# Kernel tuning notes

Hardware: AMD Instinct MI355X
Metric: run time of the kernel (lower is better)

## Reference

```python
import jax, jax.numpy as jnp
import numpy as np

DIV_VAL = 11.313708498984761  # sqrt(128), the softmax temperature used as div_val


def setup_inputs() -> dict:
    key = jax.random.key(0)
    kq, kk, kv = jax.random.split(key, 3)
    B, Lq, Lk, D = 16, 4096, 4096, 128
    return {
        "query": jax.random.normal(kq, (B, Lq, D), dtype=jnp.float32),
        "key": jax.random.normal(kk, (B, Lk, D), dtype=jnp.float32),
        "value": jax.random.normal(kv, (B, Lk, D), dtype=jnp.float32),
    }


def reference(query, key, value):
    # qk = Q @ K^T, scaled by 1/div_val  -> [B, Lq, Lk]
    scaled_qk = jnp.einsum("bqd,bkd->bqk", query, key) / DIV_VAL
    # numerically stable softmax over last axis; dropout is identity (eval / p=0)
    attn = jax.nn.softmax(scaled_qk, axis=-1)
    # output = attn @ V -> [B, Lq, Dv]
    return jnp.einsum("bqk,bkd->bqd", attn, value)
```

## Files before the change

kernel.cpp:

```cpp
#include <hip/hip_runtime.h>

#define B_  16
#define L_  4096
#define D_  128
#define NT  (L_ / 64)

typedef __attribute__((ext_vector_type(8)))  __bf16 bf16x8;
typedef __attribute__((ext_vector_type(2)))  __bf16 bf16x2;
typedef __attribute__((ext_vector_type(16))) float  f32x16;
typedef __attribute__((ext_vector_type(4)))  float  f32x4;
typedef __attribute__((ext_vector_type(4)))  int    i32x4;
typedef __attribute__((ext_vector_type(8)))  unsigned short u16x8;
typedef __attribute__((ext_vector_type(4)))  unsigned short u16x4;

#ifndef __has_builtin
#define __has_builtin(x) 0
#endif
#if __has_builtin(__builtin_amdgcn_permlane32_swap)
#define HAVE_PLSWAP 1
#else
#define HAVE_PLSWAP 0
#endif

__device__ __forceinline__ unsigned short f2bf(float f){
  unsigned u = __builtin_bit_cast(unsigned, f);
  u += 0x7fffu + ((u >> 16) & 1u);
  return (unsigned short)(u >> 16);
}

__device__ __forceinline__ int packbf(float a, float b){
  bf16x2 t; t[0] = (__bf16)a; t[1] = (__bf16)b;
  return __builtin_bit_cast(int, t);
}

__device__ __forceinline__ void gload16(const void* g, void* l){
  __builtin_amdgcn_global_load_lds(
      (const __attribute__((address_space(1))) unsigned int*)g,
      (__attribute__((address_space(3))) unsigned int*)l, 16, 0, 0);
}

__device__ __forceinline__ f32x16 z16(){
  f32x16 t;
#pragma unroll
  for (int i = 0; i < 16; ++i) t[i] = 0.f;
  return t;
}

__global__ void cvt_bf16_kernel(const float* __restrict__ in,
                                unsigned short* __restrict__ out, int n8,
                                float scale){
  int i = blockIdx.x * blockDim.x + threadIdx.x;
  if (i >= n8) return;
  const float4* p = reinterpret_cast<const float4*>(in) + (size_t)i * 2;
  float4 a = p[0], b = p[1];
  u16x8 o;
  o[0]=f2bf(a.x*scale); o[1]=f2bf(a.y*scale); o[2]=f2bf(a.z*scale); o[3]=f2bf(a.w*scale);
  o[4]=f2bf(b.x*scale); o[5]=f2bf(b.y*scale); o[6]=f2bf(b.z*scale); o[7]=f2bf(b.w*scale);
  reinterpret_cast<u16x8*>(out)[i] = o;
}

__global__ void transpose_v_kernel(const float* __restrict__ V,
                                   unsigned short* __restrict__ Vt){
  __shared__ unsigned short tile[64][65];
  const int k0 = blockIdx.x * 64, d0 = blockIdx.y * 64, b = blockIdx.z;
  const int tr = threadIdx.x >> 4, tc = threadIdx.x & 15;
  const float* src = V + ((size_t)b * L_ + k0) * D_ + d0;
#pragma unroll
  for (int p = 0; p < 4; ++p){
    int kl = p * 16 + tr;
    float4 v = *reinterpret_cast<const float4*>(src + (size_t)kl * D_ + tc * 4);
    tile[kl][tc*4+0] = f2bf(v.x);
    tile[kl][tc*4+1] = f2bf(v.y);
    tile[kl][tc*4+2] = f2bf(v.z);
    tile[kl][tc*4+3] = f2bf(v.w);
  }
  __syncthreads();
  unsigned short* dst = Vt + (size_t)b * D_ * L_ + (size_t)d0 * L_ + k0;
#pragma unroll
  for (int p = 0; p < 4; ++p){
    int dl = p * 16 + tr;
    u16x4 o;
    o[0] = tile[tc*4+0][dl];
    o[1] = tile[tc*4+1][dl];
    o[2] = tile[tc*4+2][dl];
    o[3] = tile[tc*4+3][dl];
    *reinterpret_cast<u16x4*>(dst + (size_t)dl * L_ + tc * 4) = o;
  }
}

__device__ __forceinline__ bf16x8 mkchunk(float a0,float a1,float a2,float a3,
                                          float a4,float a5,float a6,float a7,
                                          int hi){
  int x0 = packbf(a0,a1), x1 = packbf(a2,a3);
  int x2 = packbf(a4,a5), x3 = packbf(a6,a7);
  int W0, W1, W2, W3;
#if HAVE_PLSWAP
  {
    auto r = __builtin_amdgcn_permlane32_swap((unsigned)x0, (unsigned)x2, false, false);
    W0 = (int)r[0]; W2 = (int)r[1];
  }
  {
    auto r = __builtin_amdgcn_permlane32_swap((unsigned)x1, (unsigned)x3, false, false);
    W1 = (int)r[0]; W3 = (int)r[1];
  }
  (void)hi;
#else
  int y0 = __shfl_xor(x0, 32), y1 = __shfl_xor(x1, 32);
  int y2 = __shfl_xor(x2, 32), y3 = __shfl_xor(x3, 32);
  W0 = hi ? y2 : x0;  W1 = hi ? y3 : x1;
  W2 = hi ? x2 : y0;  W3 = hi ? x3 : y1;
#endif
  i32x4 ww; ww[0]=W0; ww[1]=W1; ww[2]=W2; ww[3]=W3;
  return __builtin_bit_cast(bf16x8, ww);
}

__global__ __launch_bounds__(512, 1)
void attn_kernel(const float* __restrict__ Q,
                 const unsigned short* __restrict__ Kb,
                 const unsigned short* __restrict__ Vt,
                 float* __restrict__ out){
  __shared__ char smem[131072];
  char* Klds = smem;
  char* Vlds = smem + 65536;

  const int tid = threadIdx.x;
  const int w = tid >> 6, l = tid & 63;
  const int row = l & 31, hi = l >> 5;
  const int swz = (row & 15) << 4;
  const int b = blockIdx.x, qt = blockIdx.y;

  const float* qptr = Q + ((size_t)b * L_ + (size_t)qt * 256 + w * 32 + row) * D_;
  bf16x8 qf[8];
#pragma unroll
  for (int c = 0; c < 8; ++c){
    float4 a  = *reinterpret_cast<const float4*>(qptr + c * 16 + hi * 8);
    float4 bb = *reinterpret_cast<const float4*>(qptr + c * 16 + hi * 8 + 4);
    u16x8 o;
    o[0]=f2bf(a.x);  o[1]=f2bf(a.y);  o[2]=f2bf(a.z);  o[3]=f2bf(a.w);
    o[4]=f2bf(bb.x); o[5]=f2bf(bb.y); o[6]=f2bf(bb.z); o[7]=f2bf(bb.w);
    qf[c] = __builtin_bit_cast(bf16x8, o);
  }

  const char* Kg = (const char*)(Kb + (size_t)b * L_ * D_);
  const char* Vg = (const char*)(Vt + (size_t)b * (size_t)D_ * L_);

  f32x16 o[4];
#pragma unroll
  for (int n = 0; n < 4; ++n) o[n] = z16();
  float ln = 0.f;

  auto STAGE = [&](int bsel, int t){
    char* kd = Klds + bsel * 16384;
    char* vd = Vlds + bsel * 16384;
    const int kv0 = t * 64;
#pragma unroll
    for (int j = 0; j < 2; ++j){
      int idx = j * 512 + tid;
      int kr = idx >> 4, sc = idx & 15;
      int clog = (sc << 4) ^ ((kr & 15) << 4);
      gload16(Kg + (size_t)(kv0 + kr) * 256 + clog, kd + idx * 16);
    }
#pragma unroll
    for (int j = 0; j < 2; ++j){
      int idx = j * 512 + tid;
      int lr = idx >> 4, sc = idx & 15;
      int clog = (sc << 4) ^ ((lr & 15) << 4);
      int dd = lr + ((clog >> 7) << 6);
      gload16(Vg + (size_t)dd * (L_ * 2) + (size_t)kv0 * 2 + (clog & 127),
              vd + idx * 16);
    }
  };

#define QKT(C0, C1, KC)                                                        \
  {                                                                            \
    const char* Kc_ = (KC);                                                    \
    C0 = z16(); C1 = z16();                                                    \
    __builtin_amdgcn_s_setprio(1);                                             \
    _Pragma("unroll")                                                          \
    for (int c = 0; c < 8; ++c){                                               \
      bf16x8 kf0 = *(const bf16x8*)(Kc_ + row * 256 + ((c*32 + hi*16) ^ swz)); \
      bf16x8 kf1 = *(const bf16x8*)(Kc_ + (row+32) * 256 + ((c*32 + hi*16) ^ swz)); \
      C0 = __builtin_amdgcn_mfma_f32_32x32x16_bf16(kf0, qf[c], C0, 0, 0, 0);   \
      C1 = __builtin_amdgcn_mfma_f32_32x32x16_bf16(kf1, qf[c], C1, 0, 0, 0);   \
    }                                                                          \
    __builtin_amdgcn_s_setprio(0);                                             \
  }

#define SMPACK(P0, P1)                                                         \
    _Pragma("unroll")                                                          \
    for (int i2 = 0; i2 < 16; ++i2){                                           \
      P0[i2] = __builtin_amdgcn_exp2f(P0[i2]);                                 \
      P1[i2] = __builtin_amdgcn_exp2f(P1[i2]);                                 \
    }                                                                          \
    {                                                                          \
      f32x16 pt_ = P0 + P1;                                                    \
      float a0 = pt_[0]+pt_[1],  a1 = pt_[2]+pt_[3];                           \
      float a2 = pt_[4]+pt_[5],  a3 = pt_[6]+pt_[7];                           \
      float a4 = pt_[8]+pt_[9],  a5 = pt_[10]+pt_[11];                         \
      float a6 = pt_[12]+pt_[13], a7 = pt_[14]+pt_[15];                        \
      ln += ((a0+a1)+(a2+a3)) + ((a4+a5)+(a6+a7));                             \
    }                                                                          \
    bf16x8 pa0 = mkchunk(P0[0],P0[1],P0[2],P0[3],P0[4],P0[5],P0[6],P0[7], hi); \
    bf16x8 pa1 = mkchunk(P0[8],P0[9],P0[10],P0[11],P0[12],P0[13],P0[14],P0[15], hi); \
    bf16x8 pa2 = mkchunk(P1[0],P1[1],P1[2],P1[3],P1[4],P1[5],P1[6],P1[7], hi); \
    bf16x8 pa3 = mkchunk(P1[8],P1[9],P1[10],P1[11],P1[12],P1[13],P1[14],P1[15], hi);

#define VF(VP, N, CH)                                                          \
  (*(const bf16x8*)((VP) + ((N & 1) * 32 + row) * 256 +                        \
                    ((((N >> 1) * 128) + (CH)*32 + hi*16) ^ swz)))

#define PVONLY(VP)                                                             \
  {                                                                            \
    const char* Vp_ = (VP);                                                    \
    __builtin_amdgcn_s_setprio(1);                                             \
    _Pragma("unroll")                                                          \
    for (int n2 = 0; n2 < 4; ++n2){                                            \
      bf16x8 vf0 = VF(Vp_, n2, 0);                                             \
      bf16x8 vf1 = VF(Vp_, n2, 1);                                             \
      bf16x8 vf2 = VF(Vp_, n2, 2);                                             \
      bf16x8 vf3 = VF(Vp_, n2, 3);                                             \
      o[n2] = __builtin_amdgcn_mfma_f32_32x32x16_bf16(vf0, pa0, o[n2], 0,0,0); \
      o[n2] = __builtin_amdgcn_mfma_f32_32x32x16_bf16(vf1, pa1, o[n2], 0,0,0); \
      o[n2] = __builtin_amdgcn_mfma_f32_32x32x16_bf16(vf2, pa2, o[n2], 0,0,0); \
      o[n2] = __builtin_amdgcn_mfma_f32_32x32x16_bf16(vf3, pa3, o[n2], 0,0,0); \
    }                                                                          \
    __builtin_amdgcn_s_setprio(0);                                             \
  }

#define BODY(I, C0, C1, P0, P1)                                                \
  {                                                                            \
    const int i_ = (I);                                                        \
    if (i_ + 2 < NT) STAGE((i_ + 2) & 3, i_ + 2);                              \
    SMPACK(P0, P1)                                                             \
    const char* Kc_ = Klds + (i_ & 3) * 16384;                                 \
    const char* Vp_ = Vlds + ((i_ - 1) & 3) * 16384;                           \
    C0 = z16(); C1 = z16();                                                    \
    __builtin_amdgcn_s_setprio(1);                                             \
    _Pragma("unroll")                                                          \
    for (int c = 0; c < 4; ++c){                                               \
      bf16x8 kf0a = *(const bf16x8*)(Kc_ + row * 256 + (((2*c)*32 + hi*16) ^ swz)); \
      bf16x8 kf1a = *(const bf16x8*)(Kc_ + (row+32) * 256 + (((2*c)*32 + hi*16) ^ swz)); \
      bf16x8 kf0b = *(const bf16x8*)(Kc_ + row * 256 + (((2*c+1)*32 + hi*16) ^ swz)); \
      bf16x8 kf1b = *(const bf16x8*)(Kc_ + (row+32) * 256 + (((2*c+1)*32 + hi*16) ^ swz)); \
      bf16x8 vf0 = VF(Vp_, c, 0);                                              \
      bf16x8 vf1 = VF(Vp_, c, 1);                                              \
      bf16x8 vf2 = VF(Vp_, c, 2);                                              \
      bf16x8 vf3 = VF(Vp_, c, 3);                                              \
      C0 = __builtin_amdgcn_mfma_f32_32x32x16_bf16(kf0a, qf[2*c],   C0, 0,0,0);\
      o[c] = __builtin_amdgcn_mfma_f32_32x32x16_bf16(vf0, pa0, o[c], 0,0,0);   \
      C1 = __builtin_amdgcn_mfma_f32_32x32x16_bf16(kf1a, qf[2*c],   C1, 0,0,0);\
      o[c] = __builtin_amdgcn_mfma_f32_32x32x16_bf16(vf1, pa1, o[c], 0,0,0);   \
      C0 = __builtin_amdgcn_mfma_f32_32x32x16_bf16(kf0b, qf[2*c+1], C0, 0,0,0);\
      o[c] = __builtin_amdgcn_mfma_f32_32x32x16_bf16(vf2, pa2, o[c], 0,0,0);   \
      C1 = __builtin_amdgcn_mfma_f32_32x32x16_bf16(kf1b, qf[2*c+1], C1, 0,0,0);\
      o[c] = __builtin_amdgcn_mfma_f32_32x32x16_bf16(vf3, pa3, o[c], 0,0,0);   \
    }                                                                          \
    __builtin_amdgcn_s_setprio(0);                                             \
    if (i_ + 2 < NT) { asm volatile("s_waitcnt vmcnt(4)" ::: "memory"); }      \
    else             { asm volatile("s_waitcnt vmcnt(0)" ::: "memory"); }      \
    __builtin_amdgcn_s_barrier();                                              \
  }

  STAGE(0, 0); STAGE(1, 1); STAGE(2, 2);
  asm volatile("s_waitcnt vmcnt(4)" ::: "memory");
  __builtin_amdgcn_s_barrier();

  f32x16 sA0, sA1, sB0, sB1;
  QKT(sA0, sA1, Klds);

  for (int i = 1; i <= NT - 3; i += 2){
    BODY(i,     sB0, sB1, sA0, sA1);
    BODY(i + 1, sA0, sA1, sB0, sB1);
  }
  BODY(NT - 1, sB0, sB1, sA0, sA1);
  { SMPACK(sB0, sB1) PVONLY(Vlds + ((NT - 1) & 3) * 16384); }

  float lt = ln + __shfl_xor(ln, 32);
  float inv = 1.0f / lt;
  float* outp = out + ((size_t)b * L_ + (size_t)qt * 256 + w * 32 + row) * D_;
#pragma unroll
  for (int n = 0; n < 4; ++n)
#pragma unroll
    for (int rq = 0; rq < 4; ++rq){
      f32x4 v4;
      v4[0] = o[n][rq*4+0] * inv;
      v4[1] = o[n][rq*4+1] * inv;
      v4[2] = o[n][rq*4+2] * inv;
      v4[3] = o[n][rq*4+3] * inv;
      *reinterpret_cast<f32x4*>(outp + n * 32 + rq * 8 + hi * 4) = v4;
    }
}

extern "C" void kernel_launch(void* const* d_in, const int* in_sizes, int n_in,
                              void* d_out, int out_size, void* d_ws, size_t ws_size,
                              hipStream_t stream){
  const float* Q = (const float*)d_in[0];
  const float* K = (const float*)d_in[1];
  const float* V = (const float*)d_in[2];
  float* out = (float*)d_out;

  const size_t NE = (size_t)B_ * L_ * D_;
  unsigned short* kb = (unsigned short*)d_ws;
  unsigned short* vt = kb + NE;

  const float SCALE_L2E = 1.4426950408889634f / 11.313708498984761f;
  int n8 = (int)(NE / 8);
  cvt_bf16_kernel<<<dim3(n8 / 256), 256, 0, stream>>>(K, kb, n8, SCALE_L2E);
  transpose_v_kernel<<<dim3(L_ / 64, D_ / 64, B_), 256, 0, stream>>>(V, vt);
  attn_kernel<<<dim3(B_, L_ / 256), 512, 0, stream>>>(Q, kb, vt, out);
}
```

Baseline: 172.3 us.

## Interleave softmax exp with QK^T MFMAs and reorder PV by K-chunk

Restructures the main loop body so that the exp2 and row-sum work for the previous tile is spread across the QK^T MFMA loop, four elements per step, instead of being done up front. The PV multiply now runs after QK^T and is grouped by K-chunk, so each packed P chunk is consumed right after it is built. The first QK^T MFMA seeds its accumulator from a zero constant rather than zeroing the accumulator separately. The aim is to hide VALU exp latency behind matrix-core work. In exchange, the QK and PV MFMAs are no longer interleaved, and register pressure and dependency chains shift.

```diff
diff --git a/kernel.cpp b/kernel.cpp
--- a/kernel.cpp
+++ b/kernel.cpp
@@ -147,6 +147,7 @@
   f32x16 o[4];
 #pragma unroll
   for (int n = 0; n < 4; ++n) o[n] = z16();
+  const f32x16 ZERO = z16();
   float ln = 0.f;
 
   auto STAGE = [&](int bsel, int t){
@@ -171,90 +172,60 @@
     }
   };
 
-#define QKT(C0, C1, KC)                                                        \
-  {                                                                            \
-    const char* Kc_ = (KC);                                                    \
-    C0 = z16(); C1 = z16();                                                    \
-    __builtin_amdgcn_s_setprio(1);                                             \
-    _Pragma("unroll")                                                          \
-    for (int c = 0; c < 8; ++c){                                               \
-      bf16x8 kf0 = *(const bf16x8*)(Kc_ + row * 256 + ((c*32 + hi*16) ^ swz)); \
-      bf16x8 kf1 = *(const bf16x8*)(Kc_ + (row+32) * 256 + ((c*32 + hi*16) ^ swz)); \
-      C0 = __builtin_amdgcn_mfma_f32_32x32x16_bf16(kf0, qf[c], C0, 0, 0, 0);   \
-      C1 = __builtin_amdgcn_mfma_f32_32x32x16_bf16(kf1, qf[c], C1, 0, 0, 0);   \
-    }                                                                          \
-    __builtin_amdgcn_s_setprio(0);                                             \
-  }
-
-#define SMPACK(P0, P1)                                                         \
-    _Pragma("unroll")                                                          \
-    for (int i2 = 0; i2 < 16; ++i2){                                           \
-      P0[i2] = __builtin_amdgcn_exp2f(P0[i2]);                                 \
-      P1[i2] = __builtin_amdgcn_exp2f(P1[i2]);                                 \
-    }                                                                          \
+#define SMC(P, J)                                                              \
+      P[(J)+0] = __builtin_amdgcn_exp2f(P[(J)+0]);                             \
+      P[(J)+1] = __builtin_amdgcn_exp2f(P[(J)+1]);                             \
+      P[(J)+2] = __builtin_amdgcn_exp2f(P[(J)+2]);                             \
+      P[(J)+3] = __builtin_amdgcn_exp2f(P[(J)+3]);                             \
+      ln += (P[(J)+0] + P[(J)+1]) + (P[(J)+2] + P[(J)+3]);
+
+#define KF2(KC, C)                                                             \
+      bf16x8 kf0 = *(const bf16x8*)((KC) + row * 256 + (((C)*32 + hi*16) ^ swz)); \
+      bf16x8 kf1 = *(const bf16x8*)((KC) + (row+32) * 256 + (((C)*32 + hi*16) ^ swz));
+
+#define PVG(VP, G, PA)                                                         \
     {                                                                          \
-      f32x16 pt_ = P0 + P1;                                                    \
-      float a0 = pt_[0]+pt_[1],  a1 = pt_[2]+pt_[3];                           \
-      float a2 = pt_[4]+pt_[5],  a3 = pt_[6]+pt_[7];                           \
-      float a4 = pt_[8]+pt_[9],  a5 = pt_[10]+pt_[11];                         \
-      float a6 = pt_[12]+pt_[13], a7 = pt_[14]+pt_[15];                        \
-      ln += ((a0+a1)+(a2+a3)) + ((a4+a5)+(a6+a7));                             \
-    }                                                                          \
+      bf16x8 v0 = *(const bf16x8*)((VP) + (0*32 + row) * 256 + (((G)*32 + hi*16) ^ swz));          \
+      bf16x8 v1 = *(const bf16x8*)((VP) + (1*32 + row) * 256 + (((G)*32 + hi*16) ^ swz));          \
+      bf16x8 v2 = *(const bf16x8*)((VP) + (0*32 + row) * 256 + ((128 + (G)*32 + hi*16) ^ swz));    \
+      bf16x8 v3 = *(const bf16x8*)((VP) + (1*32 + row) * 256 + ((128 + (G)*32 + hi*16) ^ swz));    \
+      o[0] = __builtin_amdgcn_mfma_f32_32x32x16_bf16(v0, PA, o[0], 0, 0, 0);   \
+      o[1] = __builtin_amdgcn_mfma_f32_32x32x16_bf16(v1, PA, o[1], 0, 0, 0);   \
+      o[2] = __builtin_amdgcn_mfma_f32_32x32x16_bf16(v2, PA, o[2], 0, 0, 0);   \
+      o[3] = __builtin_amdgcn_mfma_f32_32x32x16_bf16(v3, PA, o[3], 0, 0, 0);   \
+    }
+
+#define PVALL(VP, P0, P1)                                                      \
     bf16x8 pa0 = mkchunk(P0[0],P0[1],P0[2],P0[3],P0[4],P0[5],P0[6],P0[7], hi); \
     bf16x8 pa1 = mkchunk(P0[8],P0[9],P0[10],P0[11],P0[12],P0[13],P0[14],P0[15], hi); \
+    PVG(Vp_, 0, pa0)                                                           \
     bf16x8 pa2 = mkchunk(P1[0],P1[1],P1[2],P1[3],P1[4],P1[5],P1[6],P1[7], hi); \
-    bf16x8 pa3 = mkchunk(P1[8],P1[9],P1[10],P1[11],P1[12],P1[13],P1[14],P1[15], hi);
-
-#define VF(VP, N, CH)                                                          \
-  (*(const bf16x8*)((VP) + ((N & 1) * 32 + row) * 256 +                        \
-                    ((((N >> 1) * 128) + (CH)*32 + hi*16) ^ swz)))
-
-#define PVONLY(VP)                                                             \
-  {                                                                            \
-    const char* Vp_ = (VP);                                                    \
-    __builtin_amdgcn_s_setprio(1);                                             \
-    _Pragma("unroll")                                                          \
-    for (int n2 = 0; n2 < 4; ++n2){                                            \
-      bf16x8 vf0 = VF(Vp_, n2, 0);                                             \
-      bf16x8 vf1 = VF(Vp_, n2, 1);                                             \
-      bf16x8 vf2 = VF(Vp_, n2, 2);                                             \
-      bf16x8 vf3 = VF(Vp_, n2, 3);                                             \
-      o[n2] = __builtin_amdgcn_mfma_f32_32x32x16_bf16(vf0, pa0, o[n2], 0,0,0); \
-      o[n2] = __builtin_amdgcn_mfma_f32_32x32x16_bf16(vf1, pa1, o[n2], 0,0,0); \
-      o[n2] = __builtin_amdgcn_mfma_f32_32x32x16_bf16(vf2, pa2, o[n2], 0,0,0); \
-      o[n2] = __builtin_amdgcn_mfma_f32_32x32x16_bf16(vf3, pa3, o[n2], 0,0,0); \
-    }                                                                          \
-    __builtin_amdgcn_s_setprio(0);                                             \
-  }
+    PVG(Vp_, 1, pa1)                                                           \
+    bf16x8 pa3 = mkchunk(P1[8],P1[9],P1[10],P1[11],P1[12],P1[13],P1[14],P1[15], hi); \
+    PVG(Vp_, 2, pa2)                                                           \
+    PVG(Vp_, 3, pa3)
 
 #define BODY(I, C0, C1, P0, P1)                                                \
   {                                                                            \
     const int i_ = (I);                                                        \
     if (i_ + 2 < NT) STAGE((i_ + 2) & 3, i_ + 2);                              \
-    SMPACK(P0, P1)                                                             \
     const char* Kc_ = Klds + (i_ & 3) * 16384;                                 \
     const char* Vp_ = Vlds + ((i_ - 1) & 3) * 16384;                           \
-    C0 = z16(); C1 = z16();                                                    \
     __builtin_amdgcn_s_setprio(1);                                             \
+    {                                      \
+      KF2(Kc_, 0)                                                              \
+      C0 = __builtin_amdgcn_mfma_f32_32x32x16_bf16(kf0, qf[0], ZERO, 0, 0, 0); \
+      C1 = __builtin_amdgcn_mfma_f32_32x32x16_bf16(kf1, qf[0], ZERO, 0, 0, 0); \
+      SMC(P0, 0)                                                               \
+    }                                                                          \
     _Pragma("unroll")                                                          \
-    for (int c = 0; c < 4; ++c){                                               \
-      bf16x8 kf0a = *(const bf16x8*)(Kc_ + row * 256 + (((2*c)*32 + hi*16) ^ swz)); \
-      bf16x8 kf1a = *(const bf16x8*)(Kc_ + (row+32) * 256 + (((2*c)*32 + hi*16) ^ swz)); \
-      bf16x8 kf0b = *(const bf16x8*)(Kc_ + row * 256 + (((2*c+1)*32 + hi*16) ^ swz)); \
-      bf16x8 kf1b = *(const bf16x8*)(Kc_ + (row+32) * 256 + (((2*c+1)*32 + hi*16) ^ swz)); \
-      bf16x8 vf0 = VF(Vp_, c, 0);                                              \
-      bf16x8 vf1 = VF(Vp_, c, 1);                                              \
-      bf16x8 vf2 = VF(Vp_, c, 2);                                              \
-      bf16x8 vf3 = VF(Vp_, c, 3);                                              \
-      C0 = __builtin_amdgcn_mfma_f32_32x32x16_bf16(kf0a, qf[2*c],   C0, 0,0,0);\
-      o[c] = __builtin_amdgcn_mfma_f32_32x32x16_bf16(vf0, pa0, o[c], 0,0,0);   \
-      C1 = __builtin_amdgcn_mfma_f32_32x32x16_bf16(kf1a, qf[2*c],   C1, 0,0,0);\
-      o[c] = __builtin_amdgcn_mfma_f32_32x32x16_bf16(vf1, pa1, o[c], 0,0,0);   \
-      C0 = __builtin_amdgcn_mfma_f32_32x32x16_bf16(kf0b, qf[2*c+1], C0, 0,0,0);\
-      o[c] = __builtin_amdgcn_mfma_f32_32x32x16_bf16(vf2, pa2, o[c], 0,0,0);   \
-      C1 = __builtin_amdgcn_mfma_f32_32x32x16_bf16(kf1b, qf[2*c+1], C1, 0,0,0);\
-      o[c] = __builtin_amdgcn_mfma_f32_32x32x16_bf16(vf3, pa3, o[c], 0,0,0);   \
+    for (int c = 1; c < 8; ++c){                                               \
+      KF2(Kc_, c)                                                              \
+      C0 = __builtin_amdgcn_mfma_f32_32x32x16_bf16(kf0, qf[c], C0, 0, 0, 0);   \
+      C1 = __builtin_amdgcn_mfma_f32_32x32x16_bf16(kf1, qf[c], C1, 0, 0, 0);   \
+      if (c < 4) { SMC(P0, 4*c) } else { SMC(P1, 4*(c-4)) }                    \
     }                                                                          \
+    PVALL(Vp_, P0, P1)                                                         \
     __builtin_amdgcn_s_setprio(0);                                             \
     if (i_ + 2 < NT) { asm volatile("s_waitcnt vmcnt(4)" ::: "memory"); }      \
     else             { asm volatile("s_waitcnt vmcnt(0)" ::: "memory"); }      \
@@ -266,14 +237,38 @@
   __builtin_amdgcn_s_barrier();
 
   f32x16 sA0, sA1, sB0, sB1;
-  QKT(sA0, sA1, Klds);
+  {
+    const char* Kc_ = Klds;
+    __builtin_amdgcn_s_setprio(1);
+    {
+      KF2(Kc_, 0)
+      sA0 = __builtin_amdgcn_mfma_f32_32x32x16_bf16(kf0, qf[0], ZERO, 0, 0, 0);
+      sA1 = __builtin_amdgcn_mfma_f32_32x32x16_bf16(kf1, qf[0], ZERO, 0, 0, 0);
+    }
+#pragma unroll
+    for (int c = 1; c < 8; ++c){
+      KF2(Kc_, c)
+      sA0 = __builtin_amdgcn_mfma_f32_32x32x16_bf16(kf0, qf[c], sA0, 0, 0, 0);
+      sA1 = __builtin_amdgcn_mfma_f32_32x32x16_bf16(kf1, qf[c], sA1, 0, 0, 0);
+    }
+    __builtin_amdgcn_s_setprio(0);
+  }
 
   for (int i = 1; i <= NT - 3; i += 2){
     BODY(i,     sB0, sB1, sA0, sA1);
     BODY(i + 1, sA0, sA1, sB0, sB1);
   }
   BODY(NT - 1, sB0, sB1, sA0, sA1);
-  { SMPACK(sB0, sB1) PVONLY(Vlds + ((NT - 1) & 3) * 16384); }
+  {
+    const char* Vp_ = Vlds + ((NT - 1) & 3) * 16384;
+#pragma unroll
+    for (int j = 0; j < 16; j += 4) { SMC(sB0, j) }
+#pragma unroll
+    for (int j = 0; j < 16; j += 4) { SMC(sB1, j) }
+    __builtin_amdgcn_s_setprio(1);
+    PVALL(Vp_, sB0, sB1)
+    __builtin_amdgcn_s_setprio(0);
+  }
 
   float lt = ln + __shfl_xor(ln, 32);
   float inv = 1.0f / lt;
```

New measurement: 168.9 us. 2.0% less time.
